# Optimization experiments

Hardware: AMD Instinct MI355X
Metric: run time of the kernel (lower is better)

## Reference

```python
import jax, jax.numpy as jnp
import numpy as np

B, C, N = 8, 128, 4096
C2 = C // 2
BN_EPS = 1e-5


def setup_inputs() -> dict:
    key = jax.random.key(0)
    ks = jax.random.split(key, 8)
    s = 1.0 / np.sqrt(C)
    s2 = 1.0 / np.sqrt(C2)
    return {
        "x": jax.random.normal(ks[0], (B, C, N), dtype=jnp.float32),
        "w_qk": jax.random.uniform(ks[1], (C2, C), jnp.float32, -s, s),  # shared q/k weight
        "w_v": jax.random.uniform(ks[2], (C2, C), jnp.float32, -s, s),
        "b_v": jax.random.uniform(ks[3], (C2,), jnp.float32, -s, s),
        "w_x": jax.random.uniform(ks[4], (C2, C), jnp.float32, -s, s),
        "w_t": jax.random.uniform(ks[5], (C2, C2), jnp.float32, -s2, s2),
        "b_t": jax.random.uniform(ks[6], (C2,), jnp.float32, -s2, s2),
        "gamma": jnp.ones((C2,), jnp.float32),
        "beta": jnp.zeros((C2,), jnp.float32),
    }


def reference(x, w_qk, w_v, b_v, w_x, w_t, b_t, gamma, beta):
    # 1x1 convs are per-point linear maps: [B,C,N] -> [B,C2,N]
    x_q = jnp.einsum("oc,bcn->bno", w_qk, x)          # [B, N, C2]
    x_k = jnp.einsum("oc,bcn->bon", w_qk, x)          # [B, C2, N]
    x_v = jnp.einsum("oc,bcn->bon", w_v, x) + b_v[None, :, None]

    energy = jnp.einsum("bno,bom->bnm", x_q, x_k)     # [B, N, N]
    attn = jax.nn.softmax(energy, axis=-1)            # row softmax
    attn = attn / (1e-9 + attn.sum(axis=1, keepdims=True))  # column L1 renorm

    x_r = jnp.einsum("bon,bnm->bom", x_v, attn)       # [B, C2, N]
    x_c = jnp.einsum("oc,bcn->bon", w_x, x)           # [B, C2, N]

    d = x_c - x_r
    t = jnp.einsum("oi,bin->bon", w_t, d) + b_t[None, :, None]
    # BatchNorm1d (training-mode batch stats) over (B, N) per channel
    mean = t.mean(axis=(0, 2), keepdims=True)
    var = t.var(axis=(0, 2), keepdims=True)
    t_hat = (t - mean) * jax.lax.rsqrt(var + BN_EPS)
    x_r2 = jax.nn.relu(gamma[None, :, None] * t_hat + beta[None, :, None])
    return x_c + x_r2
```

## Files before the change

kernel.cpp:

```cpp
#include <hip/hip_runtime.h>

#define B_   8
#define C_   128
#define N_   4096
#define C2_  64

typedef __bf16 bf16x8 __attribute__((ext_vector_type(8)));
typedef float  f32x4  __attribute__((ext_vector_type(4)));

#define MFMA16(a, b, c) __builtin_amdgcn_mfma_f32_16x16x32_bf16((a), (b), (c), 0, 0, 0)

#define QK_SCALE 1.2011224087864498f

static __device__ __forceinline__ unsigned short f2bf(float f) {
    union { __bf16 b; unsigned short u; } cv;
    cv.b = (__bf16)f;
    return cv.u;
}
static __device__ __forceinline__ float bf2f(unsigned short u) {
    union { unsigned int u; float f; } cv;
    cv.u = ((unsigned int)u) << 16;
    return cv.f;
}

struct us4 { unsigned short a, b, c, d; };

static __device__ __forceinline__ void gl_lds16(const unsigned short* g, void* l) {
    __builtin_amdgcn_global_load_lds(
        (const __attribute__((address_space(1))) unsigned int*)g,
        (__attribute__((address_space(3))) unsigned int*)l,
        16, 0, 0);
}

__global__ __launch_bounds__(256) void k0_wcvt(
    const float* __restrict__ wq, const float* __restrict__ wv,
    const float* __restrict__ wx, unsigned short* __restrict__ wst)
{
    const int i4 = (blockIdx.x * 256 + threadIdx.x) * 4;
    const int mat = i4 >> 13;
    const float* src = (mat == 0) ? wq : (mat == 1) ? wv : wx;
    const float sc = (mat == 0) ? QK_SCALE : 1.0f;
    const float4 v = *(const float4*)(src + (i4 & 8191));
    us4 pk;
    pk.a = f2bf(v.x * sc); pk.b = f2bf(v.y * sc);
    pk.c = f2bf(v.z * sc); pk.d = f2bf(v.w * sc);
    *(us4*)(wst + i4) = pk;
}

__global__ __launch_bounds__(256) void k1_proj(
    const float* __restrict__ x, const unsigned short* __restrict__ wst,
    const float* __restrict__ b_v,
    unsigned short* __restrict__ qk_t, unsigned short* __restrict__ xv_bf,
    unsigned short* __restrict__ xc_bf)
{
    __shared__ __align__(16) unsigned short w_lds[192 * 128];
    __shared__ __align__(16) unsigned short x_t[64 * 136];
    const int tid = threadIdx.x;
    const int wave = tid >> 6, lane = tid & 63;
    const int quad = lane >> 4, col = lane & 15;
    const int b = blockIdx.y;
    const int n0 = blockIdx.x * 64;

    #pragma unroll
    for (int it = 0; it < 12; ++it) {
        const int idx = it * 256 + tid;
        const int row = idx >> 4, seg = idx & 15;
        gl_lds16(wst + (size_t)row * 128 + (size_t)(seg ^ (row & 7)) * 8,
                 w_lds + idx * 8);
    }
    const float* xb = x + (size_t)b * C_ * N_ + n0;
    #pragma unroll
    for (int it = 0; it < 8; ++it) {
        const int idx = it * 256 + tid;
        const int c = idx >> 4, n = (idx & 15) * 4;
        const float4 v = *(const float4*)(xb + (size_t)c * N_ + n);
        x_t[(n + 0) * 136 + c] = f2bf(v.x);
        x_t[(n + 1) * 136 + c] = f2bf(v.y);
        x_t[(n + 2) * 136 + c] = f2bf(v.z);
        x_t[(n + 3) * 136 + c] = f2bf(v.w);
    }
    __syncthreads();

    const int nw = wave * 16;
    bf16x8 bfr[4];
    #pragma unroll
    for (int kt = 0; kt < 4; ++kt)
        bfr[kt] = *(const bf16x8*)&x_t[(nw + col) * 136 + kt * 32 + quad * 8];

    const int n_g = n0 + nw + col;

    #pragma unroll
    for (int ot = 0; ot < 12; ++ot) {
        f32x4 acc = {0.f, 0.f, 0.f, 0.f};
        #pragma unroll
        for (int kt = 0; kt < 4; ++kt) {
            const bf16x8 afr = *(const bf16x8*)&w_lds[
                ((ot * 16 + col) << 7) + (((kt * 4 + quad) ^ (col & 7)) << 3)];
            acc = MFMA16(afr, bfr[kt], acc);
        }
        if (ot < 4) {
            us4 pk;
            pk.a = f2bf(acc[0]); pk.b = f2bf(acc[1]);
            pk.c = f2bf(acc[2]); pk.d = f2bf(acc[3]);
            *(us4*)&qk_t[(size_t)(b * N_ + n_g) * C2_ + ot * 16 + quad * 4] = pk;
        } else if (ot < 8) {
            const float4 bv4 = *(const float4*)(b_v + (ot - 4) * 16 + quad * 4);
            const float* bvp = (const float*)&bv4;
            #pragma unroll
            for (int r = 0; r < 4; ++r)
                xv_bf[(size_t)(b * C2_ + (ot - 4) * 16 + quad * 4 + r) * N_ + n_g]
                    = f2bf(acc[r] + bvp[r]);
        } else {
            #pragma unroll
            for (int r = 0; r < 4; ++r)
                xc_bf[(size_t)(b * C2_ + (ot - 8) * 16 + quad * 4 + r) * N_ + n_g]
                    = f2bf(acc[r]);
        }
    }
}

__global__ __launch_bounds__(256) void k2_sym(
    const unsigned short* __restrict__ qk_t, float* __restrict__ part_rs)
{
    __shared__ __align__(16) unsigned short slab[128 * 64];
    __shared__ float cwl[4 * 128];
    const int tid = threadIdx.x;
    const int wave = tid >> 6, lane = tid & 63;
    const int quad = lane >> 4, col = lane & 15;
    const int b = blockIdx.x & 7;
    int job = blockIdx.x >> 3, ti = 0;
    while (job >= 32 - ti) { job -= 32 - ti; ++ti; }
    const int tj = ti + job;
    const unsigned short* qb = qk_t + (size_t)b * N_ * C2_;

    const int n_base = ti * 128 + wave * 32;
    bf16x8 a0[2], a1[2];
    #pragma unroll
    for (int s = 0; s < 2; ++s) {
        const unsigned short* p = qb + (size_t)(n_base + s * 16 + col) * C2_ + quad * 8;
        a0[s] = *(const bf16x8*)p;
        a1[s] = *(const bf16x8*)(p + 32);
    }

    #pragma unroll
    for (int r = 0; r < 4; ++r) {
        const int idx = r * 256 + tid;
        const int row = idx >> 3, seg = idx & 7;
        gl_lds16(qb + (size_t)(tj * 128 + row) * C2_ + (size_t)(seg ^ (row & 7)) * 8,
                 slab + idx * 8);
    }
    __syncthreads();

    float run_s[2][4];
    #pragma unroll
    for (int s = 0; s < 2; ++s)
        #pragma unroll
        for (int r = 0; r < 4; ++r) run_s[s][r] = 0.f;

    #pragma unroll
    for (int g = 0; g < 8; ++g) {
        const int row = g * 16 + col;
        const bf16x8 b0 = *(const bf16x8*)(slab + row * 64 + ((quad ^ (col & 7)) * 8));
        const bf16x8 b1 = *(const bf16x8*)(slab + row * 64 + (((4 + quad) ^ (col & 7)) * 8));
        float cs = 0.f;
        #pragma unroll
        for (int s = 0; s < 2; ++s) {
            f32x4 acc = {0.f, 0.f, 0.f, 0.f};
            __builtin_amdgcn_s_setprio(1);
            acc = MFMA16(a0[s], b0, acc);
            acc = MFMA16(a1[s], b1, acc);
            __builtin_amdgcn_s_setprio(0);
            #pragma unroll
            for (int r = 0; r < 4; ++r) {
                const float u = __builtin_amdgcn_exp2f(acc[r]);
                run_s[s][r] += u;
                cs += u;
            }
        }
        cs += __shfl_xor(cs, 16, 64);
        cs += __shfl_xor(cs, 32, 64);
        if (quad == 0) cwl[wave * 128 + g * 16 + col] = cs;
    }
    __syncthreads();
    if (ti != tj && tid < 128) {
        const float c = cwl[tid] + cwl[128 + tid] + cwl[256 + tid] + cwl[384 + tid];
        part_rs[((size_t)(ti * 8 + b) << 12) + tj * 128 + tid] = c;
    }

    #pragma unroll
    for (int s = 0; s < 2; ++s)
        #pragma unroll
        for (int r = 0; r < 4; ++r) {
            #pragma unroll
            for (int off = 1; off < 16; off <<= 1)
                run_s[s][r] += __shfl_xor(run_s[s][r], off, 64);
        }
    if (col == 0) {
        #pragma unroll
        for (int s = 0; s < 2; ++s)
            #pragma unroll
            for (int r = 0; r < 4; ++r)
                part_rs[((size_t)(tj * 8 + b) << 12) + n_base + s * 16 + quad * 4 + r]
                    = run_s[s][r];
    }
}

__global__ __launch_bounds__(256) void k2w(
    const float* __restrict__ part_rs, float* __restrict__ lw)
{
    const int idx = blockIdx.x * 256 + threadIdx.x;
    const int b = idx >> 12, n = idx & 4095;
    float s = 0.f;
    #pragma unroll
    for (int t = 0; t < 32; ++t)
        s += part_rs[((size_t)(t * 8 + b) << 12) + n];
    lw[b * N_ + n] = -__log2f(s);
}

__global__ __launch_bounds__(512, 4) void k3_pv(
    const unsigned short* __restrict__ qk_t, const unsigned short* __restrict__ xv_bf,
    const float* __restrict__ lw,
    unsigned short* __restrict__ yb0, unsigned short* __restrict__ yb1,
    float* __restrict__ cspart)
{
    __shared__ __align__(16) unsigned char lds_raw[32768 + 8 * 2560];
    const int tid = threadIdx.x;
    const int wave = tid >> 6, lane = tid & 63;
    const int quad = lane >> 4, col = lane & 15;
    const int nh2 = wave & 1, mh = wave >> 1;
    const int b = blockIdx.x & 7;
    const int m_blk = ((blockIdx.x >> 3) & 31) * 128;
    const int sk = blockIdx.x >> 8;
    const int n_start = sk * 2048;
    const int n_chunks = 32;
    const int m_wave = m_blk + mh * 32;
    const unsigned short* qb = qk_t + (size_t)b * N_ * C2_;
    const unsigned short* vb = xv_bf + (size_t)b * C2_ * N_;
    const float* ln = lw + b * N_;
    unsigned short* yp = (sk == 0) ? yb0 : yb1;

    bf16x8 kb0[2], kb1[2];
    #pragma unroll
    for (int g = 0; g < 2; ++g) {
        const unsigned short* p = qb + (size_t)(m_wave + g * 16 + col) * C2_ + quad * 8;
        kb0[g] = *(const bf16x8*)p;
        kb1[g] = *(const bf16x8*)(p + 32);
    }

    bf16x8 ones;
    #pragma unroll
    for (int j = 0; j < 8; ++j) ones[j] = (__bf16)1.0f;

    unsigned short* stS = (unsigned short*)(lds_raw + 32768 + wave * 2560);

    auto stage = [&](int n0, int p) {
        unsigned char* qbase = lds_raw + p * 8192;
        unsigned char* vbase = lds_raw + 16384 + p * 8192;
        const int row = tid >> 3, seg = tid & 7;
        const int ss = seg ^ (row & 7);
        gl_lds16(qb + (size_t)(n0 + row) * C2_ + (size_t)ss * 8, qbase + tid * 16);
        gl_lds16(vb + (size_t)row * N_ + n0 + ss * 8, vbase + tid * 16);
    };

    f32x4 accY[2][4];
    #pragma unroll
    for (int g = 0; g < 2; ++g)
        #pragma unroll
        for (int os = 0; os < 4; ++os) accY[g][os] = (f32x4){0.f, 0.f, 0.f, 0.f};
    f32x4 csacc[2];
    #pragma unroll
    for (int g = 0; g < 2; ++g) csacc[g] = (f32x4){0.f, 0.f, 0.f, 0.f};

    const float* lwp = ln + n_start + nh2 * 32 + quad * 4;
    float4 lwA = *(const float4*)(lwp);
    float4 lwB = *(const float4*)(lwp + 16);

    stage(n_start, 0);
    __syncthreads();

    for (int c = 0; c < n_chunks; ++c) {
        const int n0 = n_start + c * 64;
        const int p = c & 1;
        if (c + 1 < n_chunks) stage(n0 + 64, 1 - p);

        const unsigned short* qt = (const unsigned short*)(lds_raw + p * 8192);
        const unsigned short* vt = (const unsigned short*)(lds_raw + 16384 + p * 8192);

        #pragma unroll
        for (int ns = 0; ns < 2; ++ns) {
            const int row = nh2 * 32 + ns * 16 + col;
            const bf16x8 qa0 = *(const bf16x8*)(qt + row * 64 + ((quad ^ (col & 7)) * 8));
            const bf16x8 qa1 = *(const bf16x8*)(qt + row * 64 + (((4 + quad) ^ (col & 7)) * 8));
            const float4 lw4 = ns ? lwB : lwA;
            #pragma unroll
            for (int g = 0; g < 2; ++g) {
                f32x4 acc = {lw4.x, lw4.y, lw4.z, lw4.w};
                acc = MFMA16(qa0, kb0[g], acc);
                acc = MFMA16(qa1, kb1[g], acc);
                union { unsigned short us[4]; uint2 u2; } pk;
                #pragma unroll
                for (int r = 0; r < 4; ++r)
                    pk.us[r] = f2bf(__builtin_amdgcn_exp2f(acc[r]));
                *(uint2*)&stS[(g * 16 + col) * 40 + ns * 16 + quad * 4] = pk.u2;
            }
        }

        if (c + 1 < n_chunks) {
            lwA = *(const float4*)(lwp + (c + 1) * 64);
            lwB = *(const float4*)(lwp + (c + 1) * 64 + 16);
        }

        bf16x8 sB[2];
        #pragma unroll
        for (int g = 0; g < 2; ++g)
            sB[g] = *(const bf16x8*)&stS[(g * 16 + col) * 40 + quad * 8];

        #pragma unroll
        for (int g = 0; g < 2; ++g)
            csacc[g] = MFMA16(ones, sB[g], csacc[g]);

        #pragma unroll
        for (int os = 0; os < 4; ++os) {
            const bf16x8 va = *(const bf16x8*)(vt + (os * 16 + col) * 64 +
                                               (((nh2 * 4 + quad) ^ (col & 7)) * 8));
            #pragma unroll
            for (int g = 0; g < 2; ++g)
                accY[g][os] = MFMA16(va, sB[g], accY[g][os]);
        }
        __syncthreads();
    }

    float* cmb = (float*)lds_raw;
    float* csc = (float*)(lds_raw + 32768);
    if (nh2 == 1) {
        #pragma unroll
        for (int g = 0; g < 2; ++g) {
            #pragma unroll
            for (int os = 0; os < 4; ++os)
                #pragma unroll
                for (int r = 0; r < 4; ++r)
                    cmb[((mh * 8 + g * 4 + os) * 4 + r) * 64 + lane] = accY[g][os][r];
            csc[(mh * 2 + g) * 64 + lane] = csacc[g][0];
        }
    }
    __syncthreads();
    if (nh2 == 0) {
        #pragma unroll
        for (int g = 0; g < 2; ++g) {
            const float cs = csacc[g][0] + csc[(mh * 2 + g) * 64 + lane];
            if (lane < 16)
                cspart[((size_t)sk * 8 + b) * N_ + m_wave + g * 16 + lane] = cs;
            #pragma unroll
            for (int os = 0; os < 4; ++os)
                #pragma unroll
                for (int r = 0; r < 4; ++r) {
                    const float v = accY[g][os][r] +
                        cmb[((mh * 8 + g * 4 + os) * 4 + r) * 64 + lane];
                    yp[(size_t)(b * C2_ + os * 16 + quad * 4 + r) * N_ + m_wave + g * 16 + col]
                        = f2bf(v);
                }
        }
    }
}

__global__ __launch_bounds__(256) void k4_t(
    const unsigned short* __restrict__ xc_bf, const unsigned short* __restrict__ y0,
    const unsigned short* __restrict__ y1,
    const float* __restrict__ cspart, const float* __restrict__ w_t,
    const float* __restrict__ b_t, unsigned short* __restrict__ t_bf,
    float* __restrict__ part_bn)
{
    __shared__ __align__(16) unsigned short wlds[64 * 72];
    __shared__ __align__(16) unsigned short d_t[64 * 72];
    __shared__ float cinv[64];
    const int tid = threadIdx.x;
    const int wave = tid >> 6, lane = tid & 63;
    const int quad = lane >> 4, col = lane & 15;
    const int b = blockIdx.y;
    const int n0 = blockIdx.x * 64;
    const size_t base = (size_t)b * C2_ * N_;

    #pragma unroll
    for (int it = 0; it < 4; ++it) {
        const int idx4 = it * 256 + tid;
        const int o = idx4 >> 4, i4 = (idx4 & 15) * 4;
        const float4 v = *(const float4*)(w_t + o * 64 + i4);
        us4 pk;
        pk.a = f2bf(v.x); pk.b = f2bf(v.y); pk.c = f2bf(v.z); pk.d = f2bf(v.w);
        *(us4*)&wlds[o * 72 + i4] = pk;
    }
    if (tid < 64) {
        const int n = n0 + tid;
        const float cs = cspart[(size_t)b * N_ + n] + cspart[(size_t)(8 + b) * N_ + n];
        cinv[tid] = 1.0f / (1e-9f + cs);
    }
    __syncthreads();

    #pragma unroll
    for (int it = 0; it < 4; ++it) {
        const int idx4 = it * 256 + tid;
        const int i = idx4 >> 4, n4 = (idx4 & 15) * 4;
        const size_t g = base + (size_t)i * N_ + n0 + n4;
        const us4 cx = *(const us4*)(xc_bf + g);
        const us4 u0 = *(const us4*)(y0 + g);
        const us4 u1 = *(const us4*)(y1 + g);
        d_t[(n4 + 0) * 72 + i] = f2bf(bf2f(cx.a) - (bf2f(u0.a) + bf2f(u1.a)) * cinv[n4 + 0]);
        d_t[(n4 + 1) * 72 + i] = f2bf(bf2f(cx.b) - (bf2f(u0.b) + bf2f(u1.b)) * cinv[n4 + 1]);
        d_t[(n4 + 2) * 72 + i] = f2bf(bf2f(cx.c) - (bf2f(u0.c) + bf2f(u1.c)) * cinv[n4 + 2]);
        d_t[(n4 + 3) * 72 + i] = f2bf(bf2f(cx.d) - (bf2f(u0.d) + bf2f(u1.d)) * cinv[n4 + 3]);
    }
    __syncthreads();

    const int ow = wave * 16;
    bf16x8 afr[2];
    #pragma unroll
    for (int kt = 0; kt < 2; ++kt)
        afr[kt] = *(const bf16x8*)&wlds[(ow + col) * 72 + kt * 32 + quad * 8];
    const float4 bt4 = *(const float4*)(b_t + ow + quad * 4);
    const float* btp = (const float*)&bt4;

    float s[4] = {0.f, 0.f, 0.f, 0.f}, q2[4] = {0.f, 0.f, 0.f, 0.f};
    #pragma unroll
    for (int ns = 0; ns < 4; ++ns) {
        f32x4 acc = {0.f, 0.f, 0.f, 0.f};
        #pragma unroll
        for (int kt = 0; kt < 2; ++kt) {
            const bf16x8 bfr = *(const bf16x8*)&d_t[(ns * 16 + col) * 72 + kt * 32 + quad * 8];
            acc = MFMA16(afr[kt], bfr, acc);
        }
        #pragma unroll
        for (int r = 0; r < 4; ++r) {
            const float t = acc[r] + btp[r];
            t_bf[base + (size_t)(ow + quad * 4 + r) * N_ + n0 + ns * 16 + col] = f2bf(t);
            s[r] += t;
            q2[r] += t * t;
        }
    }
    #pragma unroll
    for (int r = 0; r < 4; ++r) {
        #pragma unroll
        for (int off = 1; off < 16; off <<= 1) {
            s[r]  += __shfl_xor(s[r],  off, 64);
            q2[r] += __shfl_xor(q2[r], off, 64);
        }
    }
    if (col == 0) {
        const int blk = blockIdx.x * 8 + b;
        #pragma unroll
        for (int r = 0; r < 4; ++r) {
            part_bn[(size_t)(ow + quad * 4 + r) * 512 + blk]      = s[r];
            part_bn[(size_t)(64 + ow + quad * 4 + r) * 512 + blk] = q2[r];
        }
    }
}

__global__ __launch_bounds__(256) void k5r(
    const float* __restrict__ part_bn, float* __restrict__ bn)
{
    const int c = blockIdx.x;
    const int tid = threadIdx.x, wave = tid >> 6, lane = tid & 63;
    float s = 0.f;
    for (int j = tid; j < 512; j += 256) s += part_bn[(size_t)c * 512 + j];
    #pragma unroll
    for (int off = 1; off < 64; off <<= 1) s += __shfl_xor(s, off, 64);
    __shared__ float red[4];
    if (lane == 0) red[wave] = s;
    __syncthreads();
    if (tid == 0) bn[c] = red[0] + red[1] + red[2] + red[3];
}

__global__ __launch_bounds__(256) void k6_out(
    const unsigned short* __restrict__ xc_bf, const unsigned short* __restrict__ t_bf,
    const float* __restrict__ bn, const float* __restrict__ gamma,
    const float* __restrict__ beta, float* __restrict__ out)
{
    const int idx = blockIdx.x * 256 + threadIdx.x;
    const int o = (idx >> 10) & 63;
    const float invC = 1.0f / (float)(B_ * N_);
    const float mean = bn[o] * invC;
    const float var  = bn[64 + o] * invC - mean * mean;
    const float sc = gamma[o] * rsqrtf(var + 1e-5f);
    const float sh = beta[o] - mean * sc;
    const us4 t4 = ((const us4*)t_bf)[idx];
    const us4 c4 = ((const us4*)xc_bf)[idx];
    float4 r;
    r.x = bf2f(c4.a) + fmaxf(0.f, sc * bf2f(t4.a) + sh);
    r.y = bf2f(c4.b) + fmaxf(0.f, sc * bf2f(t4.b) + sh);
    r.z = bf2f(c4.c) + fmaxf(0.f, sc * bf2f(t4.c) + sh);
    r.w = bf2f(c4.d) + fmaxf(0.f, sc * bf2f(t4.d) + sh);
    ((float4*)out)[idx] = r;
}

extern "C" void kernel_launch(void* const* d_in, const int* in_sizes, int n_in,
                              void* d_out, int out_size, void* d_ws, size_t ws_size,
                              hipStream_t stream) {
    const float* x     = (const float*)d_in[0];
    const float* w_qk  = (const float*)d_in[1];
    const float* w_v   = (const float*)d_in[2];
    const float* b_v   = (const float*)d_in[3];
    const float* w_x   = (const float*)d_in[4];
    const float* w_t   = (const float*)d_in[5];
    const float* b_t   = (const float*)d_in[6];
    const float* gamma = (const float*)d_in[7];
    const float* beta  = (const float*)d_in[8];
    float* out = (float*)d_out;

    char* ws = (char*)d_ws;
    unsigned short* qk_t  = (unsigned short*)ws;
    unsigned short* xv_bf = (unsigned short*)(ws + (4  << 20));
    unsigned short* xc_bf = (unsigned short*)(ws + (8  << 20));
    unsigned short* t_bf  = (unsigned short*)(ws + (12 << 20));
    unsigned short* yb0 = (unsigned short*)(ws + (16 << 20));
    unsigned short* yb1 = (unsigned short*)(ws + (20 << 20));
    float* part_rs = (float*)(ws + (24 << 20));
    float* cspart  = (float*)(ws + (32 << 20));
    float* part_bn = (float*)(ws + (33 << 20));
    float* bn      = (float*)(ws + (33 << 20) + (256 << 10));
    unsigned short* wstack = (unsigned short*)d_out;
    float* lw = (float*)((char*)d_out + (256 << 10));

    hipLaunchKernelGGL(k0_wcvt,     dim3(24),     256, 0, stream, w_qk, w_v, w_x, wstack);
    hipLaunchKernelGGL(k1_proj,     dim3(64, 8),  256, 0, stream,
                       x, wstack, b_v, qk_t, xv_bf, xc_bf);
    hipLaunchKernelGGL(k2_sym,      dim3(4224),   256, 0, stream, qk_t, part_rs);
    hipLaunchKernelGGL(k2w,         dim3(128),    256, 0, stream, part_rs, lw);
    hipLaunchKernelGGL(k3_pv,       dim3(512),    512, 0, stream,
                       qk_t, xv_bf, lw, yb0, yb1, cspart);
    hipLaunchKernelGGL(k4_t,        dim3(64, 8),  256, 0, stream,
                       xc_bf, yb0, yb1, cspart, w_t, b_t, t_bf, part_bn);
    hipLaunchKernelGGL(k5r,         dim3(128),    256, 0, stream, part_bn, bn);
    hipLaunchKernelGGL(k6_out,      dim3(2048),   256, 0, stream, xc_bf, t_bf, bn, gamma, beta, out);
}
```

Baseline: 165.8 us.

## Fuse small helper kernels into neighbors to cut launch count

Removes three tiny kernels. Weight conversion now happens inside the projection kernel, the per-row log-sum reduction moves into the PV kernel's prologue via LDS, and the BN stat reduction is recomputed in every output block. This cuts launch and dependency overhead between stages. In exchange, work is duplicated: each projection block converts all weights, each PV block rereads 32 partials per row, and each of the 2048 output blocks reduces 1024 partials.

```diff
diff --git a/kernel.cpp b/kernel.cpp
--- a/kernel.cpp
+++ b/kernel.cpp
@@ -32,28 +32,14 @@
         16, 0, 0);
 }
 
-__global__ __launch_bounds__(256) void k0_wcvt(
-    const float* __restrict__ wq, const float* __restrict__ wv,
-    const float* __restrict__ wx, unsigned short* __restrict__ wst)
-{
-    const int i4 = (blockIdx.x * 256 + threadIdx.x) * 4;
-    const int mat = i4 >> 13;
-    const float* src = (mat == 0) ? wq : (mat == 1) ? wv : wx;
-    const float sc = (mat == 0) ? QK_SCALE : 1.0f;
-    const float4 v = *(const float4*)(src + (i4 & 8191));
-    us4 pk;
-    pk.a = f2bf(v.x * sc); pk.b = f2bf(v.y * sc);
-    pk.c = f2bf(v.z * sc); pk.d = f2bf(v.w * sc);
-    *(us4*)(wst + i4) = pk;
-}
-
 __global__ __launch_bounds__(256) void k1_proj(
-    const float* __restrict__ x, const unsigned short* __restrict__ wst,
-    const float* __restrict__ b_v,
+    const float* __restrict__ x, const float* __restrict__ w_qk,
+    const float* __restrict__ w_v, const float* __restrict__ b_v,
+    const float* __restrict__ w_x,
     unsigned short* __restrict__ qk_t, unsigned short* __restrict__ xv_bf,
     unsigned short* __restrict__ xc_bf)
 {
-    __shared__ __align__(16) unsigned short w_lds[192 * 128];
+    __shared__ __align__(16) unsigned short w_lds[192 * 136];
     __shared__ __align__(16) unsigned short x_t[64 * 136];
     const int tid = threadIdx.x;
     const int wave = tid >> 6, lane = tid & 63;
@@ -61,12 +47,19 @@
     const int b = blockIdx.y;
     const int n0 = blockIdx.x * 64;
 
-    #pragma unroll
-    for (int it = 0; it < 12; ++it) {
-        const int idx = it * 256 + tid;
-        const int row = idx >> 4, seg = idx & 15;
-        gl_lds16(wst + (size_t)row * 128 + (size_t)(seg ^ (row & 7)) * 8,
-                 w_lds + idx * 8);
+    const float* wsrc[3] = {w_qk, w_v, w_x};
+    #pragma unroll
+    for (int mat = 0; mat < 3; ++mat) {
+        const float* wm = wsrc[mat];
+        #pragma unroll
+        for (int it = 0; it < 8; ++it) {
+            const int idx = it * 256 + tid;
+            const int o = idx >> 5, c = (idx & 31) * 4;
+            const float4 v = *(const float4*)(wm + o * C_ + c);
+            us4 pk;
+            pk.a = f2bf(v.x); pk.b = f2bf(v.y); pk.c = f2bf(v.z); pk.d = f2bf(v.w);
+            *(us4*)&w_lds[(mat * 64 + o) * 136 + c] = pk;
+        }
     }
     const float* xb = x + (size_t)b * C_ * N_ + n0;
     #pragma unroll
@@ -94,14 +87,13 @@
         f32x4 acc = {0.f, 0.f, 0.f, 0.f};
         #pragma unroll
         for (int kt = 0; kt < 4; ++kt) {
-            const bf16x8 afr = *(const bf16x8*)&w_lds[
-                ((ot * 16 + col) << 7) + (((kt * 4 + quad) ^ (col & 7)) << 3)];
+            const bf16x8 afr = *(const bf16x8*)&w_lds[(ot * 16 + col) * 136 + kt * 32 + quad * 8];
             acc = MFMA16(afr, bfr[kt], acc);
         }
         if (ot < 4) {
             us4 pk;
-            pk.a = f2bf(acc[0]); pk.b = f2bf(acc[1]);
-            pk.c = f2bf(acc[2]); pk.d = f2bf(acc[3]);
+            pk.a = f2bf(acc[0] * QK_SCALE); pk.b = f2bf(acc[1] * QK_SCALE);
+            pk.c = f2bf(acc[2] * QK_SCALE); pk.d = f2bf(acc[3] * QK_SCALE);
             *(us4*)&qk_t[(size_t)(b * N_ + n_g) * C2_ + ot * 16 + quad * 4] = pk;
         } else if (ot < 8) {
             const float4 bv4 = *(const float4*)(b_v + (ot - 4) * 16 + quad * 4);
@@ -205,25 +197,13 @@
     }
 }
 
-__global__ __launch_bounds__(256) void k2w(
-    const float* __restrict__ part_rs, float* __restrict__ lw)
-{
-    const int idx = blockIdx.x * 256 + threadIdx.x;
-    const int b = idx >> 12, n = idx & 4095;
-    float s = 0.f;
-    #pragma unroll
-    for (int t = 0; t < 32; ++t)
-        s += part_rs[((size_t)(t * 8 + b) << 12) + n];
-    lw[b * N_ + n] = -__log2f(s);
-}
-
 __global__ __launch_bounds__(512, 4) void k3_pv(
     const unsigned short* __restrict__ qk_t, const unsigned short* __restrict__ xv_bf,
-    const float* __restrict__ lw,
+    const float* __restrict__ part_rs,
     unsigned short* __restrict__ yb0, unsigned short* __restrict__ yb1,
     float* __restrict__ cspart)
 {
-    __shared__ __align__(16) unsigned char lds_raw[32768 + 8 * 2560];
+    __shared__ __align__(16) unsigned char lds_raw[32768 + 8 * 2560 + 8192];
     const int tid = threadIdx.x;
     const int wave = tid >> 6, lane = tid & 63;
     const int quad = lane >> 4, col = lane & 15;
@@ -236,8 +216,18 @@
     const int m_wave = m_blk + mh * 32;
     const unsigned short* qb = qk_t + (size_t)b * N_ * C2_;
     const unsigned short* vb = xv_bf + (size_t)b * C2_ * N_;
-    const float* ln = lw + b * N_;
     unsigned short* yp = (sk == 0) ? yb0 : yb1;
+
+    float* lwl = (float*)(lds_raw + 53248);
+    #pragma unroll
+    for (int i = 0; i < 4; ++i) {
+        const int nl = i * 512 + tid;
+        float s = 0.f;
+        #pragma unroll
+        for (int t = 0; t < 32; ++t)
+            s += part_rs[((size_t)(t * 8 + b) << 12) + n_start + nl];
+        lwl[nl] = -__log2f(s);
+    }
 
     bf16x8 kb0[2], kb1[2];
     #pragma unroll
@@ -271,12 +261,12 @@
     #pragma unroll
     for (int g = 0; g < 2; ++g) csacc[g] = (f32x4){0.f, 0.f, 0.f, 0.f};
 
-    const float* lwp = ln + n_start + nh2 * 32 + quad * 4;
+    stage(n_start, 0);
+    __syncthreads();
+
+    const float* lwp = lwl + nh2 * 32 + quad * 4;
     float4 lwA = *(const float4*)(lwp);
     float4 lwB = *(const float4*)(lwp + 16);
-
-    stage(n_start, 0);
-    __syncthreads();
 
     for (int c = 0; c < n_chunks; ++c) {
         const int n0 = n_start + c * 64;
@@ -454,31 +444,34 @@
     }
 }
 
-__global__ __launch_bounds__(256) void k5r(
-    const float* __restrict__ part_bn, float* __restrict__ bn)
-{
-    const int c = blockIdx.x;
-    const int tid = threadIdx.x, wave = tid >> 6, lane = tid & 63;
-    float s = 0.f;
-    for (int j = tid; j < 512; j += 256) s += part_bn[(size_t)c * 512 + j];
-    #pragma unroll
-    for (int off = 1; off < 64; off <<= 1) s += __shfl_xor(s, off, 64);
-    __shared__ float red[4];
-    if (lane == 0) red[wave] = s;
-    __syncthreads();
-    if (tid == 0) bn[c] = red[0] + red[1] + red[2] + red[3];
-}
-
 __global__ __launch_bounds__(256) void k6_out(
     const unsigned short* __restrict__ xc_bf, const unsigned short* __restrict__ t_bf,
-    const float* __restrict__ bn, const float* __restrict__ gamma,
+    const float* __restrict__ part_bn, const float* __restrict__ gamma,
     const float* __restrict__ beta, float* __restrict__ out)
 {
-    const int idx = blockIdx.x * 256 + threadIdx.x;
-    const int o = (idx >> 10) & 63;
+    __shared__ float red[8];
+    const int tid = threadIdx.x, wave = tid >> 6, lane = tid & 63;
+    const int o = ((blockIdx.x * 256) >> 10) & 63;
+    float s = 0.f, q = 0.f;
+    #pragma unroll
+    for (int j = tid; j < 512; j += 256) {
+        s += part_bn[(size_t)o * 512 + j];
+        q += part_bn[(size_t)(64 + o) * 512 + j];
+    }
+    #pragma unroll
+    for (int off = 1; off < 64; off <<= 1) {
+        s += __shfl_xor(s, off, 64);
+        q += __shfl_xor(q, off, 64);
+    }
+    if (lane == 0) { red[wave] = s; red[4 + wave] = q; }
+    __syncthreads();
+    const float sum = red[0] + red[1] + red[2] + red[3];
+    const float sq  = red[4] + red[5] + red[6] + red[7];
+
+    const int idx = blockIdx.x * 256 + tid;
     const float invC = 1.0f / (float)(B_ * N_);
-    const float mean = bn[o] * invC;
-    const float var  = bn[64 + o] * invC - mean * mean;
+    const float mean = sum * invC;
+    const float var  = sq * invC - mean * mean;
     const float sc = gamma[o] * rsqrtf(var + 1e-5f);
     const float sh = beta[o] - mean * sc;
     const us4 t4 = ((const us4*)t_bf)[idx];
@@ -515,19 +508,13 @@
     float* part_rs = (float*)(ws + (24 << 20));
     float* cspart  = (float*)(ws + (32 << 20));
     float* part_bn = (float*)(ws + (33 << 20));
-    float* bn      = (float*)(ws + (33 << 20) + (256 << 10));
-    unsigned short* wstack = (unsigned short*)d_out;
-    float* lw = (float*)((char*)d_out + (256 << 10));
-
-    hipLaunchKernelGGL(k0_wcvt,     dim3(24),     256, 0, stream, w_qk, w_v, w_x, wstack);
+
     hipLaunchKernelGGL(k1_proj,     dim3(64, 8),  256, 0, stream,
-                       x, wstack, b_v, qk_t, xv_bf, xc_bf);
+                       x, w_qk, w_v, b_v, w_x, qk_t, xv_bf, xc_bf);
     hipLaunchKernelGGL(k2_sym,      dim3(4224),   256, 0, stream, qk_t, part_rs);
-    hipLaunchKernelGGL(k2w,         dim3(128),    256, 0, stream, part_rs, lw);
     hipLaunchKernelGGL(k3_pv,       dim3(512),    512, 0, stream,
-                       qk_t, xv_bf, lw, yb0, yb1, cspart);
+                       qk_t, xv_bf, part_rs, yb0, yb1, cspart);
     hipLaunchKernelGGL(k4_t,        dim3(64, 8),  256, 0, stream,
                        xc_bf, yb0, yb1, cspart, w_t, b_t, t_bf, part_bn);
-    hipLaunchKernelGGL(k5r,         dim3(128),    256, 0, stream, part_bn, bn);
-    hipLaunchKernelGGL(k6_out,      dim3(2048),   256, 0, stream, xc_bf, t_bf, bn, gamma, beta, out);
-}
+    hipLaunchKernelGGL(k6_out,      dim3(2048),   256, 0, stream, xc_bf, t_bf, part_bn, gamma, beta, out);
+}
```

After: 163.6 us. No clear change (-1.3%).
